# Kernel tuning notes

Hardware: AMD Instinct MI355X
Metric: run time of the kernel (lower is better)

## Reference

```python
import jax, jax.numpy as jnp
import numpy as np

B, S, D = 2, 2048, 2048
H = 16
HD = D // H  # 128


def setup_inputs() -> dict:
    key = jax.random.key(0)
    k1, k2, k3 = jax.random.split(key, 3)
    scale = 0.02
    return {
        "hidden_states": jax.random.normal(k1, (B, S, D), dtype=jnp.float32),
        "c_attn_w": jax.random.normal(k2, (D, 3 * D), dtype=jnp.float32) * scale,
        "c_attn_b": jnp.zeros((3 * D,), dtype=jnp.float32),
        "c_proj_w": jax.random.normal(k3, (D, D), dtype=jnp.float32) * scale,
        "c_proj_b": jnp.zeros((D,), dtype=jnp.float32),
    }


def reference(hidden_states, c_attn_w, c_attn_b, c_proj_w, c_proj_b):
    # Conv1D: x @ W + b  (W is [in, out])
    qkv = hidden_states @ c_attn_w + c_attn_b            # [B,S,3D]
    q, k, v = jnp.split(qkv, 3, axis=-1)                 # each [B,S,D]

    def split_heads(t):
        return t.reshape(B, S, H, HD).transpose(0, 2, 1, 3)  # [B,H,S,HD]

    q, k, v = split_heads(q), split_heads(k), split_heads(v)

    # scaled dot-product scores (scale_attn_weights=True)
    scores = jnp.einsum("bhqd,bhkd->bhqk", q, k) / jnp.sqrt(
        jnp.asarray(HD, dtype=q.dtype)
    )
    # causal mask (tril bias buffer)
    causal = jnp.tril(jnp.ones((S, S), dtype=bool))
    mask_value = jnp.finfo(scores.dtype).min
    scores = jnp.where(causal[None, None, :, :], scores, mask_value)

    attn = jax.nn.softmax(scores, axis=-1)               # [B,H,S,S]
    ctx = jnp.einsum("bhqk,bhkd->bhqd", attn, v)         # [B,H,S,HD]
    ctx = ctx.transpose(0, 2, 1, 3).reshape(B, S, D)      # merge heads

    out = ctx @ c_proj_w + c_proj_b                       # [B,S,D]
    return out
```

## Files before the change

### kernel.cpp

```cpp
#include <hip/hip_runtime.h>

typedef unsigned short u16;
typedef __bf16 bfx8 __attribute__((ext_vector_type(8)));
typedef float f32x4 __attribute__((ext_vector_type(4)));

#define B_ 2
#define S_ 2048
#define D_ 2048
#define H_ 16
#define HD_ 128
#define SD_ 6144

__device__ __forceinline__ u16 f2bf(float f) {
  union { float f; unsigned u; } v; v.f = f;
  unsigned r = v.u + 0x7fffu + ((v.u >> 16) & 1u);
  return (u16)(r >> 16);
}
__device__ __forceinline__ float bf2f(u16 b) {
  union { unsigned u; float f; } v; v.u = ((unsigned)b) << 16;
  return v.f;
}
__device__ __forceinline__ void gload_lds16(const void* g, void* l) {
  __builtin_amdgcn_global_load_lds((const __attribute__((address_space(1))) void*)g,
                                   (__attribute__((address_space(3))) void*)l, 16, 0, 0);
}

#define BAR() do { asm volatile("" ::: "memory"); __builtin_amdgcn_s_barrier(); \
                   asm volatile("" ::: "memory"); } while (0)
#define WAIT_VM4() asm volatile("s_waitcnt vmcnt(4)" ::: "memory")
#define WAIT_VM3() asm volatile("s_waitcnt vmcnt(3)" ::: "memory")
#define WAIT_VM0() asm volatile("s_waitcnt vmcnt(0)" ::: "memory")

__device__ __forceinline__ void tile_coords(int BM, int BN, int& m0, int& n0) {
  int flat = blockIdx.x + gridDim.x * blockIdx.y;
  int xcd = flat & 7, li = flat >> 3;
  int MW = gridDim.y >> 3;
  int half = li >> 1, nn = li & 1;
  int mloc = half % MW, nw = half / MW;
  m0 = (xcd * MW + mloc) * BM;
  n0 = (nw * 2 + nn) * BN;
}

__global__ __launch_bounds__(256) void cvt_kernel(const float* __restrict__ in,
                                                  u16* __restrict__ out, int n4) {
  int i = blockIdx.x * blockDim.x + threadIdx.x;
  int stride = gridDim.x * blockDim.x;
  for (int idx = i; idx < n4; idx += stride) {
    float4 v = ((const float4*)in)[idx];
    uint2 o;
    o.x = (unsigned)f2bf(v.x) | ((unsigned)f2bf(v.y) << 16);
    o.y = (unsigned)f2bf(v.z) | ((unsigned)f2bf(v.w) << 16);
    ((uint2*)out)[idx] = o;
  }
}

__global__ __launch_bounds__(256) void transpose_cvt(const float* __restrict__ in,
                                                     u16* __restrict__ out,
                                                     int R, int C) {
  __shared__ float tile[32][33];
  int tx = threadIdx.x, ty = threadIdx.y;
  int c0 = blockIdx.x * 32, r0 = blockIdx.y * 32;
  for (int i = 0; i < 4; ++i)
    tile[ty + i * 8][tx] = in[(size_t)(r0 + ty + i * 8) * C + c0 + tx];
  __syncthreads();
  for (int i = 0; i < 4; ++i)
    out[(size_t)(c0 + ty + i * 8) * R + r0 + tx] = f2bf(tile[tx][ty + i * 8]);
}

__global__ __launch_bounds__(256) void transpose_v(const u16* __restrict__ qkv,
                                                   u16* __restrict__ vt) {
  __shared__ u16 tile[32][33];
  int tx = threadIdx.x, ty = threadIdx.y;
  int bh = blockIdx.z;
  int b = bh >> 4, h = bh & 15;
  int s0 = blockIdx.x * 32, d0 = blockIdx.y * 32;
  const u16* src = qkv + (size_t)b * S_ * SD_ + 2 * D_ + h * HD_;
  for (int i = 0; i < 4; ++i)
    tile[ty + i * 8][tx] = src[(size_t)(s0 + ty + i * 8) * SD_ + d0 + tx];
  __syncthreads();
  u16* dst = vt + (size_t)bh * HD_ * S_;
  for (int i = 0; i < 4; ++i)
    dst[(size_t)(d0 + ty + i * 8) * S_ + s0 + tx] = tile[tx][ty + i * 8];
}

template<int OUT_BF16>
__global__ __launch_bounds__(512, 2) void gemm8p(const u16* __restrict__ A,
                                                 const u16* __restrict__ Bt,
                                                 const float* __restrict__ bias,
                                                 void* __restrict__ Cout,
                                                 int M, int N, int K) {
  __shared__ u16 lds[2][2][2][256 * 32];

  int t = threadIdx.x, l = t & 63, w = t >> 6;
  int lr = l & 15, lg = l >> 4;
  int wr = w >> 2, wc = w & 3;

  int m0, n0;
  tile_coords(256, 256, m0, n0);

  f32x4 acc[8][4];
#pragma unroll
  for (int i = 0; i < 8; ++i)
#pragma unroll
    for (int j = 0; j < 4; ++j)
#pragma unroll
      for (int r = 0; r < 4; ++r) acc[i][j][r] = 0.0f;

  int srow = t >> 2, sc = t & 3;
  const u16* As0 = A  + (size_t)(m0 + srow) * K + ((sc ^ ((srow >> 1) & 3)) * 8);
  const u16* Bs0 = Bt + (size_t)(n0 + srow) * K + ((sc ^ ((srow >> 1) & 3)) * 8);
  size_t hstep = (size_t)128 * K;

#define STG_A(BUF, KH, KOFF) do { \
    gload_lds16(As0 + (KOFF),         &lds[0][BUF][KH][t * 8]); \
    gload_lds16(As0 + hstep + (KOFF), &lds[0][BUF][KH][4096 + t * 8]); \
  } while (0)
#define STG_B(BUF, KH, KOFF) do { \
    gload_lds16(Bs0 + (KOFF),         &lds[1][BUF][KH][t * 8]); \
    gload_lds16(Bs0 + hstep + (KOFF), &lds[1][BUF][KH][4096 + t * 8]); \
  } while (0)

  int NT = K >> 6;
  int rsw = (lg ^ ((lr >> 1) & 3)) * 8;
  int arow = wr * 128 + lr;
  int brow = wc * 64 + lr;

  STG_A(0, 0, 0); STG_B(0, 0, 0); STG_A(0, 1, 32); STG_B(0, 1, 32);
  WAIT_VM4();
  BAR();

  for (int g = 0; g < NT; ++g) {
    int cb = g & 1, sb = cb ^ 1;
    int koff = (g + 1) * 64;
    bool stg = (g + 1 < NT);
    bfx8 a0[4], a1[4], bfr[4];

    if (stg) { STG_A(sb, 0, koff); STG_B(sb, 0, koff); }
#pragma unroll
    for (int i = 0; i < 4; ++i) {
      a0[i] = *(const bfx8*)&lds[0][cb][0][(arow + i * 16) * 32 + rsw];
      a1[i] = *(const bfx8*)&lds[0][cb][0][(arow + 64 + i * 16) * 32 + rsw];
    }
#pragma unroll
    for (int j = 0; j < 4; ++j)
      bfr[j] = *(const bfx8*)&lds[1][cb][0][(brow + j * 16) * 32 + rsw];
    __builtin_amdgcn_s_setprio(1);
#pragma unroll
    for (int i = 0; i < 4; ++i)
#pragma unroll
      for (int j = 0; j < 4; ++j) {
        acc[i][j]     = __builtin_amdgcn_mfma_f32_16x16x32_bf16(a0[i], bfr[j], acc[i][j], 0, 0, 0);
        acc[4 + i][j] = __builtin_amdgcn_mfma_f32_16x16x32_bf16(a1[i], bfr[j], acc[4 + i][j], 0, 0, 0);
      }
    __builtin_amdgcn_s_setprio(0);
    if (stg) WAIT_VM4(); else WAIT_VM0();
    BAR();

    if (stg) { STG_A(sb, 1, koff + 32); STG_B(sb, 1, koff + 32); }
#pragma unroll
    for (int i = 0; i < 4; ++i) {
      a0[i] = *(const bfx8*)&lds[0][cb][1][(arow + i * 16) * 32 + rsw];
      a1[i] = *(const bfx8*)&lds[0][cb][1][(arow + 64 + i * 16) * 32 + rsw];
    }
#pragma unroll
    for (int j = 0; j < 4; ++j)
      bfr[j] = *(const bfx8*)&lds[1][cb][1][(brow + j * 16) * 32 + rsw];
    __builtin_amdgcn_s_setprio(1);
#pragma unroll
    for (int i = 0; i < 4; ++i)
#pragma unroll
      for (int j = 0; j < 4; ++j) {
        acc[i][j]     = __builtin_amdgcn_mfma_f32_16x16x32_bf16(a0[i], bfr[j], acc[i][j], 0, 0, 0);
        acc[4 + i][j] = __builtin_amdgcn_mfma_f32_16x16x32_bf16(a1[i], bfr[j], acc[4 + i][j], 0, 0, 0);
      }
    __builtin_amdgcn_s_setprio(0);
    if (stg) WAIT_VM4(); else WAIT_VM0();
    BAR();
  }
#undef STG_A
#undef STG_B

  for (int i = 0; i < 8; ++i) {
    int row = m0 + wr * 128 + i * 16 + lg * 4;
    for (int j = 0; j < 4; ++j) {
      int col = n0 + wc * 64 + j * 16 + lr;
      float bz = bias[col];
      for (int r = 0; r < 4; ++r) {
        float v = acc[i][j][r] + bz;
        if (OUT_BF16)
          ((u16*)Cout)[(size_t)(row + r) * N + col] = f2bf(v);
        else
          ((float*)Cout)[(size_t)(row + r) * N + col] = v;
      }
    }
  }
}

template<int OUT_BF16>
__global__ __launch_bounds__(512, 2) void gemm2p(const u16* __restrict__ A,
                                                 const u16* __restrict__ Bt,
                                                 const float* __restrict__ bias,
                                                 void* __restrict__ Cout,
                                                 int M, int N, int K) {
  __shared__ u16 ldsA[2][2][128 * 32];
  __shared__ u16 ldsB[2][2][256 * 32];

  int t = threadIdx.x, l = t & 63, w = t >> 6;
  int lr = l & 15, lg = l >> 4;
  int wr = w >> 2, wc = w & 3;

  int m0, n0;
  tile_coords(128, 256, m0, n0);

  f32x4 acc[4][4];
#pragma unroll
  for (int i = 0; i < 4; ++i)
#pragma unroll
    for (int j = 0; j < 4; ++j)
#pragma unroll
      for (int r = 0; r < 4; ++r) acc[i][j][r] = 0.0f;

  int srow = t >> 2, sc = t & 3;
  int csw = (sc ^ ((srow >> 1) & 3)) * 8;
  const u16* As0 = A  + (size_t)(m0 + srow) * K + csw;
  const u16* Bs0 = Bt + (size_t)(n0 + srow) * K + csw;
  size_t hstep = (size_t)128 * K;

#define STG_A(BUF, KH, KOFF) \
    gload_lds16(As0 + (KOFF), &ldsA[BUF][KH][t * 8])
#define STG_B(BUF, KH, KOFF) do { \
    gload_lds16(Bs0 + (KOFF),         &ldsB[BUF][KH][t * 8]); \
    gload_lds16(Bs0 + hstep + (KOFF), &ldsB[BUF][KH][4096 + t * 8]); \
  } while (0)

  int NT = K >> 6;
  int rsw = (lg ^ ((lr >> 1) & 3)) * 8;
  int arow = wr * 64 + lr;
  int brow = wc * 64 + lr;

  STG_A(0, 0, 0); STG_B(0, 0, 0); STG_A(0, 1, 32); STG_B(0, 1, 32);
  WAIT_VM3();
  BAR();

  for (int g = 0; g < NT; ++g) {
    int cb = g & 1, sb = cb ^ 1;
    int koff = (g + 1) * 64;
    bool stg = (g + 1 < NT);
    bfx8 af[4], bfr[4];

    if (stg) { STG_A(sb, 0, koff); STG_B(sb, 0, koff); }
#pragma unroll
    for (int i = 0; i < 4; ++i)
      af[i] = *(const bfx8*)&ldsA[cb][0][(arow + i * 16) * 32 + rsw];
#pragma unroll
    for (int j = 0; j < 4; ++j)
      bfr[j] = *(const bfx8*)&ldsB[cb][0][(brow + j * 16) * 32 + rsw];
    __builtin_amdgcn_s_setprio(1);
#pragma unroll
    for (int i = 0; i < 4; ++i)
#pragma unroll
      for (int j = 0; j < 4; ++j)
        acc[i][j] = __builtin_amdgcn_mfma_f32_16x16x32_bf16(af[i], bfr[j], acc[i][j], 0, 0, 0);
    __builtin_amdgcn_s_setprio(0);
    if (stg) WAIT_VM3(); else WAIT_VM0();
    BAR();

    if (stg) { STG_A(sb, 1, koff + 32); STG_B(sb, 1, koff + 32); }
#pragma unroll
    for (int i = 0; i < 4; ++i)
      af[i] = *(const bfx8*)&ldsA[cb][1][(arow + i * 16) * 32 + rsw];
#pragma unroll
    for (int j = 0; j < 4; ++j)
      bfr[j] = *(const bfx8*)&ldsB[cb][1][(brow + j * 16) * 32 + rsw];
    __builtin_amdgcn_s_setprio(1);
#pragma unroll
    for (int i = 0; i < 4; ++i)
#pragma unroll
      for (int j = 0; j < 4; ++j)
        acc[i][j] = __builtin_amdgcn_mfma_f32_16x16x32_bf16(af[i], bfr[j], acc[i][j], 0, 0, 0);
    __builtin_amdgcn_s_setprio(0);
    if (stg) WAIT_VM3();
    BAR();
  }
#undef STG_A
#undef STG_B

  for (int i = 0; i < 4; ++i) {
    int row = m0 + wr * 64 + i * 16 + lg * 4;
    for (int j = 0; j < 4; ++j) {
      int col = n0 + wc * 64 + j * 16 + lr;
      float bz = bias[col];
      for (int r = 0; r < 4; ++r) {
        float v = acc[i][j][r] + bz;
        if (OUT_BF16)
          ((u16*)Cout)[(size_t)(row + r) * N + col] = f2bf(v);
        else
          ((float*)Cout)[(size_t)(row + r) * N + col] = v;
      }
    }
  }
}

#define STAGE(BUF, KT) do {                                                        \
    int kc_ = ((t & 15) ^ ((t >> 4) & 7)) * 8;                                     \
    for (int i_ = 0; i_ < 4; ++i_)                                                 \
      gload_lds16(kbase + (size_t)((KT) * 64 + i_ * 16 + (t >> 4)) * SD_ + kc_,    \
                  &Klds[BUF][i_ * 2048 + t * 8]);                                  \
    int vc_ = (KT) * 64 + (((t & 7) ^ ((t >> 3) & 7)) * 8);                        \
    for (int i_ = 0; i_ < 4; ++i_)                                                 \
      gload_lds16(vbase + (size_t)(i_ * 32 + (t >> 3)) * S_ + vc_,                 \
                  &Vlds[BUF][i_ * 2048 + t * 8]);                                  \
  } while (0)

__global__ __launch_bounds__(256) void attn_kernel(const u16* __restrict__ qkv,
                                                   const u16* __restrict__ vt,
                                                   u16* __restrict__ ctx) {
  __shared__ u16 Klds[2][64 * 128];
  __shared__ u16 Vlds[2][128 * 64];
  __shared__ u16 Plds[4][16 * 64];

  int t = threadIdx.x, l = t & 63, w = t >> 6;
  int lr = l & 15, lg = l >> 4;
  int sw = lr & 7;
  int bid = blockIdx.x;
  int pr = bid >> 5, bh = bid & 31;
  int b = bh >> 4, h = bh & 15;
  const float scale = 0.08838834764831845f;

  const u16* kbase = qkv + (size_t)b * S_ * SD_ + D_ + h * HD_;
  const u16* vbase = vt + (size_t)bh * HD_ * S_;

  for (int sgi = 0; sgi < 2; ++sgi) {
    int qt = sgi ? pr : (31 - pr);
    int q0 = qt * 64;
    int wbase = q0 + w * 16;
    int nt = qt + 1;

    bfx8 qf[4];
    {
      const u16* qbase = qkv + (size_t)(b * S_ + wbase) * SD_ + h * HD_;
      for (int kk = 0; kk < 4; ++kk) {
        const u16* src = qbase + (size_t)lr * SD_ + kk * 32 + lg * 8;
        union { uint4 u; u16 s[8]; bfx8 bv; } iv, ov;
        iv.u = *(const uint4*)src;
        for (int j = 0; j < 8; ++j) ov.s[j] = f2bf(bf2f(iv.s[j]) * scale);
        qf[kk] = ov.bv;
      }
    }

    f32x4 o[8];
    float mrun = -INFINITY, lrun = 0.0f;
    for (int ht = 0; ht < 8; ++ht)
      for (int r = 0; r < 4; ++r) o[ht][r] = 0.0f;

    if (sgi) __syncthreads();
    STAGE(0, 0);

    for (int kt = 0; kt < nt; ++kt) {
      int cur = kt & 1;
      __syncthreads();
      if (kt + 1 < nt) STAGE(cur ^ 1, kt + 1);

      int kb0 = kt * 64;

      f32x4 sacc[4];
      for (int n = 0; n < 4; ++n)
        for (int r = 0; r < 4; ++r) sacc[n][r] = 0.0f;
      __builtin_amdgcn_s_setprio(1);
      for (int n = 0; n < 4; ++n) {
        bfx8 kf[4];
        int krow = n * 16 + lr;
        for (int kk = 0; kk < 4; ++kk)
          kf[kk] = *(const bfx8*)&Klds[cur][krow * 128 + ((kk * 4 + lg) ^ sw) * 8];
        for (int kk = 0; kk < 4; ++kk)
          sacc[n] = __builtin_amdgcn_mfma_f32_16x16x32_bf16(kf[kk], qf[kk], sacc[n], 0, 0, 0);
      }
      __builtin_amdgcn_s_setprio(0);

      int q = wbase + lr;
      if (kb0 + 63 > wbase) {
        for (int n = 0; n < 4; ++n)
          for (int r = 0; r < 4; ++r)
            if (kb0 + n * 16 + lg * 4 + r > q) sacc[n][r] = -INFINITY;
      }
      float tm = -INFINITY;
      for (int n = 0; n < 4; ++n) {
        float a = fmaxf(fmaxf(sacc[n][0], sacc[n][1]),
                        fmaxf(sacc[n][2], sacc[n][3]));
        tm = fmaxf(tm, a);
      }
      tm = fmaxf(tm, __shfl_xor(tm, 16, 64));
      tm = fmaxf(tm, __shfl_xor(tm, 32, 64));
      float mold = mrun;
      float mnew = fmaxf(mold, tm);
      if (__any((int)(mnew > mold))) {
        float corr = __expf(mold - mnew);
        lrun *= corr;
        mrun = mnew;
        for (int r = 0; r < 4; ++r) {
          float c = __shfl(corr, lg * 4 + r, 16);
          for (int ht = 0; ht < 8; ++ht) o[ht][r] *= c;
        }
      }
      float mm = mrun;
      float psum = 0.0f;
      for (int n = 0; n < 4; ++n) {
        float p0 = __expf(sacc[n][0] - mm);
        float p1 = __expf(sacc[n][1] - mm);
        float p2 = __expf(sacc[n][2] - mm);
        float p3 = __expf(sacc[n][3] - mm);
        psum += (p0 + p1) + (p2 + p3);
        uint2 pk;
        pk.x = (unsigned)f2bf(p0) | ((unsigned)f2bf(p1) << 16);
        pk.y = (unsigned)f2bf(p2) | ((unsigned)f2bf(p3) << 16);
        *(uint2*)&Plds[w][lr * 64 + ((n * 2 + (lg >> 1)) ^ sw) * 8 + (lg & 1) * 4] = pk;
      }
      psum += __shfl_xor(psum, 16, 64);
      psum += __shfl_xor(psum, 32, 64);
      lrun += psum;

      __builtin_amdgcn_s_setprio(1);
      for (int kk = 0; kk < 2; ++kk) {
        bfx8 pa = *(const bfx8*)&Plds[w][lr * 64 + ((kk * 4 + lg) ^ sw) * 8];
        for (int ht = 0; ht < 8; ++ht) {
          bfx8 vb = *(const bfx8*)&Vlds[cur][(ht * 16 + lr) * 64 + ((kk * 4 + lg) ^ sw) * 8];
          o[ht] = __builtin_amdgcn_mfma_f32_16x16x32_bf16(pa, vb, o[ht], 0, 0, 0);
        }
      }
      __builtin_amdgcn_s_setprio(0);
    }

    for (int r = 0; r < 4; ++r) {
      float inv = 1.0f / __shfl(lrun, lg * 4 + r, 16);
      int qa = wbase + lg * 4 + r;
      u16* dst = ctx + (size_t)(b * S_ + qa) * D_ + h * HD_;
      for (int ht = 0; ht < 8; ++ht)
        dst[ht * 16 + lr] = f2bf(o[ht][r] * inv);
    }
  }
}

extern "C" void kernel_launch(void* const* d_in, const int* in_sizes, int n_in,
                              void* d_out, int out_size, void* d_ws, size_t ws_size,
                              hipStream_t stream) {
  const float* hs     = (const float*)d_in[0];
  const float* w_attn = (const float*)d_in[1];
  const float* b_attn = (const float*)d_in[2];
  const float* w_proj = (const float*)d_in[3];
  const float* b_proj = (const float*)d_in[4];

  u16* Xb     = (u16*)d_ws;
  u16* Wqkvt  = Xb     + 8388608;
  u16* Wprojt = Wqkvt  + 12582912;
  u16* qkvb   = Wprojt + 4194304;
  u16* Vt     = qkvb   + 25165824;
  u16* ctxb   = Vt     + 8388608;

  cvt_kernel<<<2048, 256, 0, stream>>>(hs, Xb, (B_ * S_ * D_) / 4);
  transpose_cvt<<<dim3(192, 64), dim3(32, 8), 0, stream>>>(w_attn, Wqkvt, D_, 3 * D_);
  transpose_cvt<<<dim3(64, 64), dim3(32, 8), 0, stream>>>(w_proj, Wprojt, D_, D_);
  gemm8p<1><<<dim3(24, 16), 512, 0, stream>>>(Xb, Wqkvt, b_attn, qkvb, 4096, 6144, 2048);
  transpose_v<<<dim3(64, 4, 32), dim3(32, 8), 0, stream>>>(qkvb, Vt);
  attn_kernel<<<dim3(512), 256, 0, stream>>>(qkvb, Vt, ctxb);
  gemm2p<0><<<dim3(8, 32), 512, 0, stream>>>(ctxb, Wprojt, b_proj, d_out, 4096, 2048, 2048);
}
```

Before: 279.4 us.

## Switch 256x256 GEMM to 32x32x16 MFMA and reorder staging in gemm2p

```diff
diff --git a/kernel.cpp b/kernel.cpp
--- a/kernel.cpp
+++ b/kernel.cpp
@@ -3,6 +3,7 @@
 typedef unsigned short u16;
 typedef __bf16 bfx8 __attribute__((ext_vector_type(8)));
 typedef float f32x4 __attribute__((ext_vector_type(4)));
+typedef float f32x16 __attribute__((ext_vector_type(16)));
 
 #define B_ 2
 #define S_ 2048
@@ -92,19 +93,19 @@
   __shared__ u16 lds[2][2][2][256 * 32];
 
   int t = threadIdx.x, l = t & 63, w = t >> 6;
-  int lr = l & 15, lg = l >> 4;
+  int r5 = l & 31, h = l >> 5;
   int wr = w >> 2, wc = w & 3;
 
   int m0, n0;
   tile_coords(256, 256, m0, n0);
 
-  f32x4 acc[8][4];
-#pragma unroll
-  for (int i = 0; i < 8; ++i)
-#pragma unroll
-    for (int j = 0; j < 4; ++j)
-#pragma unroll
-      for (int r = 0; r < 4; ++r) acc[i][j][r] = 0.0f;
+  f32x16 acc[4][2];
+#pragma unroll
+  for (int mi = 0; mi < 4; ++mi)
+#pragma unroll
+    for (int nj = 0; nj < 2; ++nj)
+#pragma unroll
+      for (int r = 0; r < 16; ++r) acc[mi][nj][r] = 0.0f;
 
   int srow = t >> 2, sc = t & 3;
   const u16* As0 = A  + (size_t)(m0 + srow) * K + ((sc ^ ((srow >> 1) & 3)) * 8);
@@ -121,79 +122,74 @@
   } while (0)
 
   int NT = K >> 6;
-  int rsw = (lg ^ ((lr >> 1) & 3)) * 8;
-  int arow = wr * 128 + lr;
-  int brow = wc * 64 + lr;
+  int sw32 = (r5 >> 1) & 3;
+  int c0 = (0 | h) ^ sw32;
+  int c1 = (2 | h) ^ sw32;
+  int arow32 = wr * 128 + r5;
+  int brow32 = wc * 64 + r5;
 
   STG_A(0, 0, 0); STG_B(0, 0, 0); STG_A(0, 1, 32); STG_B(0, 1, 32);
   WAIT_VM4();
   BAR();
+
+#define PHASE(KH, STGSTMT, WAITSTMT) do {                                          \
+    bfx8 af[4][2], bfv[2][2];                                                      \
+    STGSTMT;                                                                       \
+    _Pragma("unroll")                                                              \
+    for (int mi = 0; mi < 4; ++mi) {                                               \
+      af[mi][0] = *(const bfx8*)&lds[0][cb][KH][(arow32 + mi * 32) * 32 + c0 * 8]; \
+      af[mi][1] = *(const bfx8*)&lds[0][cb][KH][(arow32 + mi * 32) * 32 + c1 * 8]; \
+    }                                                                              \
+    _Pragma("unroll")                                                              \
+    for (int nj = 0; nj < 2; ++nj) {                                               \
+      bfv[nj][0] = *(const bfx8*)&lds[1][cb][KH][(brow32 + nj * 32) * 32 + c0 * 8];\
+      bfv[nj][1] = *(const bfx8*)&lds[1][cb][KH][(brow32 + nj * 32) * 32 + c1 * 8];\
+    }                                                                              \
+    __builtin_amdgcn_s_setprio(1);                                                 \
+    _Pragma("unroll")                                                              \
+    for (int ks = 0; ks < 2; ++ks)                                                 \
+      _Pragma("unroll")                                                            \
+      for (int mi = 0; mi < 4; ++mi)                                               \
+        _Pragma("unroll")                                                          \
+        for (int nj = 0; nj < 2; ++nj)                                             \
+          acc[mi][nj] = __builtin_amdgcn_mfma_f32_32x32x16_bf16(af[mi][ks], bfv[nj][ks], acc[mi][nj], 0, 0, 0); \
+    __builtin_amdgcn_s_setprio(0);                                                 \
+    WAITSTMT;                                                                      \
+    BAR();                                                                         \
+  } while (0)
 
   for (int g = 0; g < NT; ++g) {
     int cb = g & 1, sb = cb ^ 1;
     int koff = (g + 1) * 64;
     bool stg = (g + 1 < NT);
-    bfx8 a0[4], a1[4], bfr[4];
-
-    if (stg) { STG_A(sb, 0, koff); STG_B(sb, 0, koff); }
-#pragma unroll
-    for (int i = 0; i < 4; ++i) {
-      a0[i] = *(const bfx8*)&lds[0][cb][0][(arow + i * 16) * 32 + rsw];
-      a1[i] = *(const bfx8*)&lds[0][cb][0][(arow + 64 + i * 16) * 32 + rsw];
-    }
-#pragma unroll
-    for (int j = 0; j < 4; ++j)
-      bfr[j] = *(const bfx8*)&lds[1][cb][0][(brow + j * 16) * 32 + rsw];
-    __builtin_amdgcn_s_setprio(1);
-#pragma unroll
-    for (int i = 0; i < 4; ++i)
-#pragma unroll
-      for (int j = 0; j < 4; ++j) {
-        acc[i][j]     = __builtin_amdgcn_mfma_f32_16x16x32_bf16(a0[i], bfr[j], acc[i][j], 0, 0, 0);
-        acc[4 + i][j] = __builtin_amdgcn_mfma_f32_16x16x32_bf16(a1[i], bfr[j], acc[4 + i][j], 0, 0, 0);
-      }
-    __builtin_amdgcn_s_setprio(0);
-    if (stg) WAIT_VM4(); else WAIT_VM0();
-    BAR();
-
-    if (stg) { STG_A(sb, 1, koff + 32); STG_B(sb, 1, koff + 32); }
-#pragma unroll
-    for (int i = 0; i < 4; ++i) {
-      a0[i] = *(const bfx8*)&lds[0][cb][1][(arow + i * 16) * 32 + rsw];
-      a1[i] = *(const bfx8*)&lds[0][cb][1][(arow + 64 + i * 16) * 32 + rsw];
-    }
-#pragma unroll
-    for (int j = 0; j < 4; ++j)
-      bfr[j] = *(const bfx8*)&lds[1][cb][1][(brow + j * 16) * 32 + rsw];
-    __builtin_amdgcn_s_setprio(1);
-#pragma unroll
-    for (int i = 0; i < 4; ++i)
-#pragma unroll
-      for (int j = 0; j < 4; ++j) {
-        acc[i][j]     = __builtin_amdgcn_mfma_f32_16x16x32_bf16(a0[i], bfr[j], acc[i][j], 0, 0, 0);
-        acc[4 + i][j] = __builtin_amdgcn_mfma_f32_16x16x32_bf16(a1[i], bfr[j], acc[4 + i][j], 0, 0, 0);
-      }
-    __builtin_amdgcn_s_setprio(0);
-    if (stg) WAIT_VM4(); else WAIT_VM0();
-    BAR();
+
+    PHASE(0,
+          if (stg) { STG_A(sb, 0, koff); STG_B(sb, 0, koff); },
+          if (stg) WAIT_VM4(); else WAIT_VM0());
+    PHASE(1,
+          if (stg) { STG_A(sb, 1, koff + 32); STG_B(sb, 1, koff + 32); },
+          if (stg) WAIT_VM4(); else WAIT_VM0());
   }
+#undef PHASE
 #undef STG_A
 #undef STG_B
 
-  for (int i = 0; i < 8; ++i) {
-    int row = m0 + wr * 128 + i * 16 + lg * 4;
-    for (int j = 0; j < 4; ++j) {
-      int col = n0 + wc * 64 + j * 16 + lr;
+#pragma unroll
+  for (int mi = 0; mi < 4; ++mi)
+#pragma unroll
+    for (int nj = 0; nj < 2; ++nj) {
+      int col = n0 + wc * 64 + nj * 32 + r5;
       float bz = bias[col];
-      for (int r = 0; r < 4; ++r) {
-        float v = acc[i][j][r] + bz;
+#pragma unroll
+      for (int r = 0; r < 16; ++r) {
+        int row = m0 + wr * 128 + mi * 32 + (r & 3) + 8 * (r >> 2) + 4 * h;
+        float v = acc[mi][nj][r] + bz;
         if (OUT_BF16)
-          ((u16*)Cout)[(size_t)(row + r) * N + col] = f2bf(v);
+          ((u16*)Cout)[(size_t)row * N + col] = f2bf(v);
         else
-          ((float*)Cout)[(size_t)(row + r) * N + col] = v;
+          ((float*)Cout)[(size_t)row * N + col] = v;
       }
     }
-  }
 }
 
 template<int OUT_BF16>
@@ -248,13 +244,14 @@
     bool stg = (g + 1 < NT);
     bfx8 af[4], bfr[4];
 
-    if (stg) { STG_A(sb, 0, koff); STG_B(sb, 0, koff); }
 #pragma unroll
     for (int i = 0; i < 4; ++i)
       af[i] = *(const bfx8*)&ldsA[cb][0][(arow + i * 16) * 32 + rsw];
 #pragma unroll
     for (int j = 0; j < 4; ++j)
       bfr[j] = *(const bfx8*)&ldsB[cb][0][(brow + j * 16) * 32 + rsw];
+    if (stg) { STG_A(sb, 0, koff); STG_B(sb, 0, koff); }
+    BAR();
     __builtin_amdgcn_s_setprio(1);
 #pragma unroll
     for (int i = 0; i < 4; ++i)
@@ -265,13 +262,14 @@
     if (stg) WAIT_VM3(); else WAIT_VM0();
     BAR();
 
-    if (stg) { STG_A(sb, 1, koff + 32); STG_B(sb, 1, koff + 32); }
 #pragma unroll
     for (int i = 0; i < 4; ++i)
       af[i] = *(const bfx8*)&ldsA[cb][1][(arow + i * 16) * 32 + rsw];
 #pragma unroll
     for (int j = 0; j < 4; ++j)
       bfr[j] = *(const bfx8*)&ldsB[cb][1][(brow + j * 16) * 32 + rsw];
+    if (stg) { STG_A(sb, 1, koff + 32); STG_B(sb, 1, koff + 32); }
+    BAR();
     __builtin_amdgcn_s_setprio(1);
 #pragma unroll
     for (int i = 0; i < 4; ++i)
```

Measured after the change: 279.8 us. About the same (+0.1%).
